# Performance work log

Measured on AMD Instinct MI355X. Metric: run time of the kernel, lower is better.

Reference implementation:

```python
import jax, jax.numpy as jnp
import numpy as np

N = 50000
E = 800000
DIN = 256
DH = 256
DOUT = 256
R = 8
B = 4


def setup_inputs() -> dict:
    key = jax.random.key(0)
    ks = jax.random.split(key, 12)
    s = 0.05
    return {
        "x": jax.random.normal(ks[0], (N, DIN), jnp.float32),
        "edge_index": jax.random.randint(ks[1], (2, E), 0, N, jnp.int64),
        "edge_type": jax.random.randint(ks[2], (E,), 0, R, jnp.int64),
        "basis1": jax.random.normal(ks[3], (B, DIN, DH), jnp.float32) * s,
        "comp1": jax.random.normal(ks[4], (R, B), jnp.float32) * s,
        "root1": jax.random.normal(ks[5], (DIN, DH), jnp.float32) * s,
        "bias1": jnp.zeros((DH,), jnp.float32),
        "basis2": jax.random.normal(ks[6], (B, DH, DOUT), jnp.float32) * s,
        "comp2": jax.random.normal(ks[7], (R, B), jnp.float32) * s,
        "root2": jax.random.normal(ks[8], (DH, DOUT), jnp.float32) * s,
        "bias2": jnp.zeros((DOUT,), jnp.float32),
    }


def rgcn_conv(x, src, dst, edge_type, basis, comp, root, bias):
    # Basis-decomposed relational conv (PyG RGCNConv, aggr='mean').
    # xb: per-node transform by each basis matrix -> [N, B, out]
    xb = jnp.einsum('ni,bio->nbo', x, basis)
    # Per-edge message: mix bases with relation coefficients -> [E, out]
    msg = jnp.einsum('eb,ebo->eo', comp[edge_type], xb[src])
    # Mean aggregation per (dst, relation): divide each edge by the count of
    # edges of its relation arriving at its destination, then scatter-add.
    key = dst * R + edge_type
    cnt = jax.ops.segment_sum(jnp.ones((msg.shape[0],), x.dtype), key,
                              num_segments=x.shape[0] * R)
    norm = 1.0 / jnp.maximum(cnt, 1.0)
    agg = jax.ops.segment_sum(msg * norm[key][:, None], dst,
                              num_segments=x.shape[0])
    return agg + x @ root + bias


def reference(x, edge_index, edge_type, basis1, comp1, root1, bias1,
              basis2, comp2, root2, bias2):
    src, dst = edge_index[0], edge_index[1]
    h = rgcn_conv(x, src, dst, edge_type, basis1, comp1, root1, bias1)
    h = jax.nn.relu(h)
    # dropout(p=0.4) is identity in eval mode
    out = rgcn_conv(h, src, dst, edge_type, basis2, comp2, root2, bias2)
    return out
```

## Files before the change

### kernel.cpp

```cpp
#include <hip/hip_runtime.h>
#include <hip/hip_bf16.h>

constexpr int N_NODES = 50000;
constexpr int N_EDGES = 800000;
constexpr int R_REL   = 8;
constexpr int BASES   = 4;
constexpr int D       = 256;
constexpr int KT      = BASES * D + D;

typedef __attribute__((ext_vector_type(8))) short bf16x8;
typedef __attribute__((ext_vector_type(4))) float f32x4;

__device__ inline float bfu_lo(unsigned u) { return __uint_as_float(u << 16); }
__device__ inline float bfu_hi(unsigned u) { return __uint_as_float(u & 0xFFFF0000u); }
__device__ inline unsigned short f2bu(float f) {
  __hip_bfloat16 h = __float2bfloat16(f);
  return *reinterpret_cast<unsigned short*>(&h);
}
__device__ inline void store_out(float* p, float v) { *p = v; }
__device__ inline void store_out(__hip_bfloat16* p, float v) { *p = __float2bfloat16(v); }

__device__ inline void gload_lds16(void* lds, const void* g) {
  __builtin_amdgcn_global_load_lds(
      (const __attribute__((address_space(1))) unsigned*)g,
      (__attribute__((address_space(3))) unsigned*)lds, 16, 0, 0);
}

__global__ __launch_bounds__(256) void count_kernel(
    const int* __restrict__ ei, const int* __restrict__ et,
    int* __restrict__ cnt) {
  int e = blockIdx.x * 256 + threadIdx.x;
  if (e < N_EDGES) {
    int dst = ei[N_EDGES + e];
    int rt  = et[e];
    atomicAdd(&cnt[dst * R_REL + rt], 1);
  }
}

__global__ __launch_bounds__(256) void scan_phaseA(
    const int* __restrict__ cnt, int* __restrict__ bsum) {
  __shared__ int sd[256];
  int tid = threadIdx.x;
  int n = blockIdx.x * 256 + tid;
  int d = 0;
  if (n < N_NODES) {
#pragma unroll
    for (int r = 0; r < R_REL; r++) d += cnt[n * R_REL + r];
  }
  sd[tid] = d;
  __syncthreads();
  for (int off = 128; off > 0; off >>= 1) {
    if (tid < off) sd[tid] += sd[tid + off];
    __syncthreads();
  }
  if (tid == 0) bsum[blockIdx.x] = sd[0];
}

__global__ __launch_bounds__(256) void scan_phaseB(
    const int* __restrict__ bsum, int* __restrict__ boff,
    int* __restrict__ estart, int NB) {
  __shared__ int sd[256];
  int tid = threadIdx.x;
  int v = (tid < NB) ? bsum[tid] : 0;
  sd[tid] = v;
  __syncthreads();
  for (int off = 1; off < 256; off <<= 1) {
    int t = (tid >= off) ? sd[tid - off] : 0;
    __syncthreads();
    sd[tid] += t;
    __syncthreads();
  }
  if (tid < NB) boff[tid] = sd[tid] - v;
  if (tid == 0) estart[N_NODES] = N_EDGES;
}

__global__ __launch_bounds__(256) void scan_phaseC(
    const int* __restrict__ cnt, const int* __restrict__ boff,
    int* __restrict__ estart) {
  __shared__ int sd[256];
  int tid = threadIdx.x;
  int n = blockIdx.x * 256 + tid;
  int d = 0;
  if (n < N_NODES) {
#pragma unroll
    for (int r = 0; r < R_REL; r++) d += cnt[n * R_REL + r];
  }
  sd[tid] = d;
  __syncthreads();
  for (int off = 1; off < 256; off <<= 1) {
    int t = (tid >= off) ? sd[tid - off] : 0;
    __syncthreads();
    sd[tid] += t;
    __syncthreads();
  }
  if (n < N_NODES) estart[n] = boff[blockIdx.x] + sd[tid] - d;
}

__global__ __launch_bounds__(256) void bucket_kernel(
    const int* __restrict__ ei, const int* __restrict__ et,
    const int* __restrict__ estart, int* __restrict__ cursor,
    int* __restrict__ packed) {
  int e = blockIdx.x * 256 + threadIdx.x;
  if (e < N_EDGES) {
    int src = ei[e];
    int dst = ei[N_EDGES + e];
    int rt  = et[e];
    int pos = estart[dst] + atomicAdd(&cursor[dst], 1);
    packed[pos] = src | (rt << 20);
  }
}

__global__ __launch_bounds__(256) void convert_kernel(
    const float* __restrict__ x, unsigned* __restrict__ x2) {
  int idx = blockIdx.x * 256 + threadIdx.x;
  if (idx < N_NODES * 128) {
    float2 v = *(const float2*)(x + (size_t)idx * 2);
    x2[idx] = (unsigned)f2bu(v.x) | ((unsigned)f2bu(v.y) << 16);
  }
}

__global__ __launch_bounds__(256) void winv_kernel(
    const int* __restrict__ cnt, const float* __restrict__ comp,
    float4* __restrict__ wtab) {
  int idx = blockIdx.x * 256 + threadIdx.x;
  if (idx < N_NODES * R_REL) {
    int r = idx & 7;
    int c = cnt[idx];
    float inv = 1.0f / (float)(c > 0 ? c : 1);
    float4 w;
    w.x = comp[r * BASES + 0] * inv;
    w.y = comp[r * BASES + 1] * inv;
    w.z = comp[r * BASES + 2] * inv;
    w.w = comp[r * BASES + 3] * inv;
    wtab[idx] = w;
  }
}

__global__ __launch_bounds__(256) void make_w_kernel(
    const float* __restrict__ basis, const float* __restrict__ root,
    __hip_bfloat16* __restrict__ WT) {
  __shared__ __hip_bfloat16 tile[64][256];
  int k0 = blockIdx.x * 64;
  int tid = threadIdx.x;
#pragma unroll 4
  for (int r = 0; r < 64; r++) {
    int k = k0 + r;
    const float* srow = (k < BASES * D)
        ? basis + ((size_t)(k & 3) * D + (k >> 2)) * D
        : root + (size_t)(k - BASES * D) * D;
    tile[r][tid] = __float2bfloat16(srow[tid]);
  }
  __syncthreads();
  __hip_bfloat16* dst = WT + (size_t)tid * KT + k0;
#pragma unroll
  for (int c = 0; c < 8; c++) {
    union { short s[8]; int4 v; } u;
#pragma unroll
    for (int r = 0; r < 8; r++)
      u.s[r] = *reinterpret_cast<short*>(&tile[c * 8 + r][tid]);
    *(int4*)(dst + c * 8) = u.v;
  }
}

__device__ inline void edge_fma(float acc[BASES][4], uint2 v, float4 w) {
  float a0 = bfu_lo(v.x), a1 = bfu_hi(v.x), a2 = bfu_lo(v.y), a3 = bfu_hi(v.y);
  acc[0][0] += w.x * a0; acc[0][1] += w.x * a1; acc[0][2] += w.x * a2; acc[0][3] += w.x * a3;
  acc[1][0] += w.y * a0; acc[1][1] += w.y * a1; acc[1][2] += w.y * a2; acc[1][3] += w.y * a3;
  acc[2][0] += w.z * a0; acc[2][1] += w.z * a1; acc[2][2] += w.z * a2; acc[2][3] += w.z * a3;
  acc[3][0] += w.w * a0; acc[3][1] += w.w * a1; acc[3][2] += w.w * a2; acc[3][3] += w.w * a3;
}

__global__ __launch_bounds__(256) void aggregate_kernel(
    const unsigned* __restrict__ x2,
    const int* __restrict__ packed,
    const int* __restrict__ estart,
    const float4* __restrict__ wtab,
    __hip_bfloat16* __restrict__ zA)
{
  int tid = threadIdx.x;
  int wave = tid >> 6, lane = tid & 63;
  int n = blockIdx.x * 4 + wave;
  const float4 wzero = make_float4(0.f, 0.f, 0.f, 0.f);

  float acc[BASES][4] = {};
  int s = estart[n], e = estart[n + 1];
  const float4* wt = wtab + (size_t)n * R_REL;

  for (int base = s; base < e; base += 4) {
    int rem = e - base;
    int i1 = base + (rem > 1 ? 1 : 0);
    int i2 = base + (rem > 2 ? 2 : 0);
    int i3 = base + (rem > 3 ? 3 : 0);
    int p0 = packed[base];
    int p1 = packed[i1];
    int p2 = packed[i2];
    int p3 = packed[i3];
    uint2 v0 = *(const uint2*)(x2 + (size_t)(p0 & 0xFFFFF) * 128 + lane * 2);
    uint2 v1 = *(const uint2*)(x2 + (size_t)(p1 & 0xFFFFF) * 128 + lane * 2);
    uint2 v2 = *(const uint2*)(x2 + (size_t)(p2 & 0xFFFFF) * 128 + lane * 2);
    uint2 v3 = *(const uint2*)(x2 + (size_t)(p3 & 0xFFFFF) * 128 + lane * 2);
    float4 w0 = wt[p0 >> 20];
    float4 w1 = (rem > 1) ? wt[p1 >> 20] : wzero;
    float4 w2 = (rem > 2) ? wt[p2 >> 20] : wzero;
    float4 w3 = (rem > 3) ? wt[p3 >> 20] : wzero;
    edge_fma(acc, v0, w0);
    edge_fma(acc, v1, w1);
    edge_fma(acc, v2, w2);
    edge_fma(acc, v3, w3);
  }

  union { short s[8]; int4 v; } u0, u1;
#pragma unroll
  for (int j = 0; j < 2; j++)
#pragma unroll
    for (int b = 0; b < BASES; b++) {
      u0.s[4 * j + b] = (short)f2bu(acc[b][j]);
      u1.s[4 * j + b] = (short)f2bu(acc[b][j + 2]);
    }
  __hip_bfloat16* zrow = zA + (size_t)n * KT;
  *(int4*)(zrow + 16 * lane) = u0.v;
  *(int4*)(zrow + 16 * lane + 8) = u1.v;

  uint2 sv = *(const uint2*)(x2 + (size_t)n * 128 + lane * 2);
  *(uint2*)((unsigned*)(zrow + BASES * D) + lane * 2) = sv;
}

#define BM 128
#define BN 256
#define BK 32

template <bool RELU, typename OutT>
__global__ __launch_bounds__(512) void gemm_kernel(
    const __hip_bfloat16* __restrict__ A,
    const __hip_bfloat16* __restrict__ Bt,
    const float* __restrict__ bias, OutT* __restrict__ C, int M) {
  __shared__ __align__(16) __hip_bfloat16 As[BM * BK];
  __shared__ __align__(16) __hip_bfloat16 Bs[BN * BK];
  int tid = threadIdx.x;
  int m0 = blockIdx.x * BM;
  int wave = tid >> 6, lane = tid & 63;
  int wm = wave & 1, wn = wave >> 1;
  int l15 = lane & 15, quad = lane >> 4;

  int colS = (lane & 3) * 8;
  int rowA = wave * 16 + (lane >> 2);
  int grA  = min(m0 + rowA, M - 1);
  const __hip_bfloat16* gA  = A + (size_t)grA * KT + colS;
  const __hip_bfloat16* gB0 = Bt + (size_t)(wave * 32 + (lane >> 2)) * KT + colS;
  const __hip_bfloat16* gB1 = gB0 + 16 * KT;
  __hip_bfloat16* lA  = As + wave * 512;
  __hip_bfloat16* lB0 = Bs + wave * 1024;
  __hip_bfloat16* lB1 = Bs + wave * 1024 + 512;

  f32x4 acc[4][4] = {};

  for (int k0 = 0; k0 < KT; k0 += BK) {
    gload_lds16(lA, gA + k0);
    gload_lds16(lB0, gB0 + k0);
    gload_lds16(lB1, gB1 + k0);
    __syncthreads();

    bf16x8 af[4], bfr[4];
#pragma unroll
    for (int mt = 0; mt < 4; mt++)
      af[mt] = *(const bf16x8*)(As + (wm * 64 + mt * 16 + l15) * BK + quad * 8);
#pragma unroll
    for (int nt = 0; nt < 4; nt++)
      bfr[nt] = *(const bf16x8*)(Bs + (wn * 64 + nt * 16 + l15) * BK + quad * 8);
#pragma unroll
    for (int mt = 0; mt < 4; mt++)
#pragma unroll
      for (int nt = 0; nt < 4; nt++)
        acc[mt][nt] = __builtin_amdgcn_mfma_f32_16x16x32_bf16(
            af[mt], bfr[nt], acc[mt][nt], 0, 0, 0);
    __syncthreads();
  }

#pragma unroll
  for (int nt = 0; nt < 4; nt++) {
    int cg = wn * 64 + nt * 16 + l15;
    float bv = bias[cg];
#pragma unroll
    for (int mt = 0; mt < 4; mt++) {
#pragma unroll
      for (int r = 0; r < 4; r++) {
        int rg = m0 + wm * 64 + mt * 16 + quad * 4 + r;
        if (rg < M) {
          float v = acc[mt][nt][r] + bv;
          if (RELU) v = fmaxf(v, 0.f);
          store_out(C + (size_t)rg * D + cg, v);
        }
      }
    }
  }
}

static inline char* carve(char*& p, size_t bytes) {
  char* r = p;
  p += (bytes + 255) & ~(size_t)255;
  return r;
}

extern "C" void kernel_launch(void* const* d_in, const int* in_sizes, int n_in,
                              void* d_out, int out_size, void* d_ws,
                              size_t ws_size, hipStream_t stream) {
  const float* x      = (const float*)d_in[0];
  const int*   ei     = (const int*)d_in[1];
  const int*   et     = (const int*)d_in[2];
  const float* basis1 = (const float*)d_in[3];
  const float* comp1  = (const float*)d_in[4];
  const float* root1  = (const float*)d_in[5];
  const float* bias1  = (const float*)d_in[6];
  const float* basis2 = (const float*)d_in[7];
  const float* comp2  = (const float*)d_in[8];
  const float* root2  = (const float*)d_in[9];
  const float* bias2  = (const float*)d_in[10];
  float* out = (float*)d_out;

  char* ws = (char*)d_ws;
  int* cnt    = (int*)carve(ws, (size_t)N_NODES * R_REL * 4);
  int* estart = (int*)carve(ws, (size_t)(N_NODES + 1) * 4);
  int* cursor = (int*)carve(ws, (size_t)N_NODES * 4);
  int* bsum   = (int*)carve(ws, 256 * 4);
  int* boff   = (int*)carve(ws, 256 * 4);
  int* packed = (int*)carve(ws, (size_t)N_EDGES * 4);
  float4* wtab1 = (float4*)carve(ws, (size_t)N_NODES * R_REL * 16);
  float4* wtab2 = (float4*)carve(ws, (size_t)N_NODES * R_REL * 16);
  __hip_bfloat16* WT1 = (__hip_bfloat16*)carve(ws, (size_t)D * KT * 2);
  __hip_bfloat16* WT2 = (__hip_bfloat16*)carve(ws, (size_t)D * KT * 2);
  unsigned* xb = (unsigned*)carve(ws, (size_t)N_NODES * D * 2);
  __hip_bfloat16* h = (__hip_bfloat16*)carve(ws, (size_t)N_NODES * D * 2);
  __hip_bfloat16* zA = (__hip_bfloat16*)carve(ws, (size_t)N_NODES * KT * 2);

  const int NB = (N_NODES + 255) / 256;
  const int EB = (N_EDGES + 255) / 256;
  const int CB = (N_NODES * 128 + 255) / 256;
  const int WB = (N_NODES * R_REL + 255) / 256;

  hipMemsetAsync(cnt, 0, (size_t)N_NODES * R_REL * 4, stream);
  hipMemsetAsync(cursor, 0, (size_t)N_NODES * 4, stream);

  count_kernel<<<EB, 256, 0, stream>>>(ei, et, cnt);
  scan_phaseA<<<NB, 256, 0, stream>>>(cnt, bsum);
  scan_phaseB<<<1, 256, 0, stream>>>(bsum, boff, estart, NB);
  scan_phaseC<<<NB, 256, 0, stream>>>(cnt, boff, estart);
  bucket_kernel<<<EB, 256, 0, stream>>>(ei, et, estart, cursor, packed);

  convert_kernel<<<CB, 256, 0, stream>>>(x, xb);
  winv_kernel<<<WB, 256, 0, stream>>>(cnt, comp1, wtab1);
  winv_kernel<<<WB, 256, 0, stream>>>(cnt, comp2, wtab2);
  make_w_kernel<<<KT / 64, 256, 0, stream>>>(basis1, root1, WT1);
  make_w_kernel<<<KT / 64, 256, 0, stream>>>(basis2, root2, WT2);

  dim3 ggrid((N_NODES + BM - 1) / BM, 1);
  const int AB = (N_NODES + 3) / 4;

  aggregate_kernel<<<AB, 256, 0, stream>>>(xb, packed, estart, wtab1, zA);
  gemm_kernel<true, __hip_bfloat16><<<ggrid, 512, 0, stream>>>(zA, WT1, bias1, h, N_NODES);

  aggregate_kernel<<<AB, 256, 0, stream>>>((const unsigned*)h, packed, estart, wtab2, zA);
  gemm_kernel<false, float><<<ggrid, 512, 0, stream>>>(zA, WT2, bias2, out, N_NODES);
}
```

Baseline: 498.4 us.

## Read self features directly in GEMM and use persistent work-stealing aggregation

The aggregation kernel no longer copies each node's own features into the concatenated A matrix. The GEMM instead reads the last K-slice straight from the node feature buffer, which removes a write and re-read of N×256 bf16 per layer. Aggregation becomes a persistent kernel: each wave takes a static chunk of nodes, then grabs more through an atomic counter, and the tail edges are handled by a scalar loop instead of masked duplicate loads. Outputs are written with nontemporal stores. This adds an atomic per chunk and a branch in the GEMM's A-pointer selection.

Result: slower. 729.5 us (+46.4%).

```diff
diff --git a/kernel.cpp b/kernel.cpp
--- a/kernel.cpp
+++ b/kernel.cpp
@@ -6,10 +6,12 @@
 constexpr int R_REL   = 8;
 constexpr int BASES   = 4;
 constexpr int D       = 256;
-constexpr int KT      = BASES * D + D;
+constexpr int KZ      = BASES * D;
+constexpr int KT      = KZ + D;
 
 typedef __attribute__((ext_vector_type(8))) short bf16x8;
 typedef __attribute__((ext_vector_type(4))) float f32x4;
+typedef __attribute__((ext_vector_type(4))) int   i32x4;
 
 __device__ inline float bfu_lo(unsigned u) { return __uint_as_float(u << 16); }
 __device__ inline float bfu_hi(unsigned u) { return __uint_as_float(u & 0xFFFF0000u); }
@@ -17,7 +19,7 @@
   __hip_bfloat16 h = __float2bfloat16(f);
   return *reinterpret_cast<unsigned short*>(&h);
 }
-__device__ inline void store_out(float* p, float v) { *p = v; }
+__device__ inline void store_out(float* p, float v) { __builtin_nontemporal_store(v, p); }
 __device__ inline void store_out(__hip_bfloat16* p, float v) { *p = __float2bfloat16(v); }
 
 __device__ inline void gload_lds16(void* lds, const void* g) {
@@ -145,9 +147,9 @@
 #pragma unroll 4
   for (int r = 0; r < 64; r++) {
     int k = k0 + r;
-    const float* srow = (k < BASES * D)
+    const float* srow = (k < KZ)
         ? basis + ((size_t)(k & 3) * D + (k >> 2)) * D
-        : root + (size_t)(k - BASES * D) * D;
+        : root + (size_t)(k - KZ) * D;
     tile[r][tid] = __float2bfloat16(srow[tid]);
   }
   __syncthreads();
@@ -162,12 +164,24 @@
   }
 }
 
-__device__ inline void edge_fma(float acc[BASES][4], uint2 v, float4 w) {
-  float a0 = bfu_lo(v.x), a1 = bfu_hi(v.x), a2 = bfu_lo(v.y), a3 = bfu_hi(v.y);
-  acc[0][0] += w.x * a0; acc[0][1] += w.x * a1; acc[0][2] += w.x * a2; acc[0][3] += w.x * a3;
-  acc[1][0] += w.y * a0; acc[1][1] += w.y * a1; acc[1][2] += w.y * a2; acc[1][3] += w.y * a3;
-  acc[2][0] += w.z * a0; acc[2][1] += w.z * a1; acc[2][2] += w.z * a2; acc[2][3] += w.z * a3;
-  acc[3][0] += w.w * a0; acc[3][1] += w.w * a1; acc[3][2] += w.w * a2; acc[3][3] += w.w * a3;
+constexpr int AGG_BLOCKS = 2048;
+constexpr int AGG_WAVES  = AGG_BLOCKS * 4;
+constexpr int GRAB       = 4;
+constexpr int NSTATIC    = AGG_WAVES * GRAB;
+
+__device__ inline float2 pfma(float s, float2 a, float2 c) {
+  c.x = fmaf(s, a.x, c.x);
+  c.y = fmaf(s, a.y, c.y);
+  return c;
+}
+
+__device__ inline void edge_fma(float2 acc[BASES][2], uint2 v, float4 w) {
+  float2 a01 = make_float2(bfu_lo(v.x), bfu_hi(v.x));
+  float2 a23 = make_float2(bfu_lo(v.y), bfu_hi(v.y));
+  acc[0][0] = pfma(w.x, a01, acc[0][0]); acc[0][1] = pfma(w.x, a23, acc[0][1]);
+  acc[1][0] = pfma(w.y, a01, acc[1][0]); acc[1][1] = pfma(w.y, a23, acc[1][1]);
+  acc[2][0] = pfma(w.z, a01, acc[2][0]); acc[2][1] = pfma(w.z, a23, acc[2][1]);
+  acc[3][0] = pfma(w.w, a01, acc[3][0]); acc[3][1] = pfma(w.w, a23, acc[3][1]);
 }
 
 __global__ __launch_bounds__(256) void aggregate_kernel(
@@ -175,54 +189,66 @@
     const int* __restrict__ packed,
     const int* __restrict__ estart,
     const float4* __restrict__ wtab,
-    __hip_bfloat16* __restrict__ zA)
+    __hip_bfloat16* __restrict__ zA,
+    int* __restrict__ wq)
 {
-  int tid = threadIdx.x;
+  int tid  = threadIdx.x;
   int wave = tid >> 6, lane = tid & 63;
-  int n = blockIdx.x * 4 + wave;
-  const float4 wzero = make_float4(0.f, 0.f, 0.f, 0.f);
-
-  float acc[BASES][4] = {};
-  int s = estart[n], e = estart[n + 1];
-  const float4* wt = wtab + (size_t)n * R_REL;
-
-  for (int base = s; base < e; base += 4) {
-    int rem = e - base;
-    int i1 = base + (rem > 1 ? 1 : 0);
-    int i2 = base + (rem > 2 ? 2 : 0);
-    int i3 = base + (rem > 3 ? 3 : 0);
-    int p0 = packed[base];
-    int p1 = packed[i1];
-    int p2 = packed[i2];
-    int p3 = packed[i3];
-    uint2 v0 = *(const uint2*)(x2 + (size_t)(p0 & 0xFFFFF) * 128 + lane * 2);
-    uint2 v1 = *(const uint2*)(x2 + (size_t)(p1 & 0xFFFFF) * 128 + lane * 2);
-    uint2 v2 = *(const uint2*)(x2 + (size_t)(p2 & 0xFFFFF) * 128 + lane * 2);
-    uint2 v3 = *(const uint2*)(x2 + (size_t)(p3 & 0xFFFFF) * 128 + lane * 2);
-    float4 w0 = wt[p0 >> 20];
-    float4 w1 = (rem > 1) ? wt[p1 >> 20] : wzero;
-    float4 w2 = (rem > 2) ? wt[p2 >> 20] : wzero;
-    float4 w3 = (rem > 3) ? wt[p3 >> 20] : wzero;
-    edge_fma(acc, v0, w0);
-    edge_fma(acc, v1, w1);
-    edge_fma(acc, v2, w2);
-    edge_fma(acc, v3, w3);
-  }
-
-  union { short s[8]; int4 v; } u0, u1;
-#pragma unroll
-  for (int j = 0; j < 2; j++)
-#pragma unroll
-    for (int b = 0; b < BASES; b++) {
-      u0.s[4 * j + b] = (short)f2bu(acc[b][j]);
-      u1.s[4 * j + b] = (short)f2bu(acc[b][j + 2]);
+  int nbase = (blockIdx.x * 4 + wave) * GRAB;
+
+  while (nbase < N_NODES) {
+    int nend = nbase + GRAB;
+    if (nend > N_NODES) nend = N_NODES;
+
+    for (int n = nbase; n < nend; n++) {
+      float2 acc[BASES][2] = {};
+      int s = estart[n], e = estart[n + 1];
+      const float4* wt = wtab + (size_t)n * R_REL;
+
+      int i = s;
+      for (; i + 4 <= e; i += 4) {
+        int p0 = packed[i];
+        int p1 = packed[i + 1];
+        int p2 = packed[i + 2];
+        int p3 = packed[i + 3];
+        uint2 v0 = *(const uint2*)(x2 + (size_t)(p0 & 0xFFFFF) * 128 + lane * 2);
+        uint2 v1 = *(const uint2*)(x2 + (size_t)(p1 & 0xFFFFF) * 128 + lane * 2);
+        uint2 v2 = *(const uint2*)(x2 + (size_t)(p2 & 0xFFFFF) * 128 + lane * 2);
+        uint2 v3 = *(const uint2*)(x2 + (size_t)(p3 & 0xFFFFF) * 128 + lane * 2);
+        float4 w0 = wt[p0 >> 20];
+        float4 w1 = wt[p1 >> 20];
+        float4 w2 = wt[p2 >> 20];
+        float4 w3 = wt[p3 >> 20];
+        edge_fma(acc, v0, w0);
+        edge_fma(acc, v1, w1);
+        edge_fma(acc, v2, w2);
+        edge_fma(acc, v3, w3);
+      }
+      for (; i < e; i++) {
+        int p = packed[i];
+        uint2 v = *(const uint2*)(x2 + (size_t)(p & 0xFFFFF) * 128 + lane * 2);
+        float4 w = wt[p >> 20];
+        edge_fma(acc, v, w);
+      }
+
+      union { short s[8]; i32x4 v; } u0, u1;
+#pragma unroll
+      for (int b = 0; b < BASES; b++) {
+        u0.s[b]     = (short)f2bu(acc[b][0].x);
+        u0.s[4 + b] = (short)f2bu(acc[b][0].y);
+        u1.s[b]     = (short)f2bu(acc[b][1].x);
+        u1.s[4 + b] = (short)f2bu(acc[b][1].y);
+      }
+      __hip_bfloat16* zrow = zA + (size_t)n * KZ;
+      __builtin_nontemporal_store(u0.v, (i32x4*)(zrow + 16 * lane));
+      __builtin_nontemporal_store(u1.v, (i32x4*)(zrow + 16 * lane + 8));
     }
-  __hip_bfloat16* zrow = zA + (size_t)n * KT;
-  *(int4*)(zrow + 16 * lane) = u0.v;
-  *(int4*)(zrow + 16 * lane + 8) = u1.v;
-
-  uint2 sv = *(const uint2*)(x2 + (size_t)n * 128 + lane * 2);
-  *(uint2*)((unsigned*)(zrow + BASES * D) + lane * 2) = sv;
+
+    int idx0 = 0;
+    if (lane == 0) idx0 = atomicAdd(wq, 1);
+    int idx = __builtin_amdgcn_readfirstlane(idx0);
+    nbase = NSTATIC + idx * GRAB;
+  }
 }
 
 #define BM 128
@@ -231,7 +257,8 @@
 
 template <bool RELU, typename OutT>
 __global__ __launch_bounds__(512) void gemm_kernel(
-    const __hip_bfloat16* __restrict__ A,
+    const __hip_bfloat16* __restrict__ Az,
+    const __hip_bfloat16* __restrict__ Aself,
     const __hip_bfloat16* __restrict__ Bt,
     const float* __restrict__ bias, OutT* __restrict__ C, int M) {
   __shared__ __align__(16) __hip_bfloat16 As[BM * BK];
@@ -245,7 +272,8 @@
   int colS = (lane & 3) * 8;
   int rowA = wave * 16 + (lane >> 2);
   int grA  = min(m0 + rowA, M - 1);
-  const __hip_bfloat16* gA  = A + (size_t)grA * KT + colS;
+  const __hip_bfloat16* gAz = Az + (size_t)grA * KZ + colS;
+  const __hip_bfloat16* gAs = Aself + (size_t)grA * D + colS;
   const __hip_bfloat16* gB0 = Bt + (size_t)(wave * 32 + (lane >> 2)) * KT + colS;
   const __hip_bfloat16* gB1 = gB0 + 16 * KT;
   __hip_bfloat16* lA  = As + wave * 512;
@@ -255,7 +283,8 @@
   f32x4 acc[4][4] = {};
 
   for (int k0 = 0; k0 < KT; k0 += BK) {
-    gload_lds16(lA, gA + k0);
+    const __hip_bfloat16* srcA = (k0 < KZ) ? (gAz + k0) : (gAs + (k0 - KZ));
+    gload_lds16(lA, srcA);
     gload_lds16(lB0, gB0 + k0);
     gload_lds16(lB1, gB1 + k0);
     __syncthreads();
@@ -323,6 +352,7 @@
   int* cursor = (int*)carve(ws, (size_t)N_NODES * 4);
   int* bsum   = (int*)carve(ws, 256 * 4);
   int* boff   = (int*)carve(ws, 256 * 4);
+  int* wq     = (int*)carve(ws, 2 * 4);
   int* packed = (int*)carve(ws, (size_t)N_EDGES * 4);
   float4* wtab1 = (float4*)carve(ws, (size_t)N_NODES * R_REL * 16);
   float4* wtab2 = (float4*)carve(ws, (size_t)N_NODES * R_REL * 16);
@@ -330,7 +360,7 @@
   __hip_bfloat16* WT2 = (__hip_bfloat16*)carve(ws, (size_t)D * KT * 2);
   unsigned* xb = (unsigned*)carve(ws, (size_t)N_NODES * D * 2);
   __hip_bfloat16* h = (__hip_bfloat16*)carve(ws, (size_t)N_NODES * D * 2);
-  __hip_bfloat16* zA = (__hip_bfloat16*)carve(ws, (size_t)N_NODES * KT * 2);
+  __hip_bfloat16* zA = (__hip_bfloat16*)carve(ws, (size_t)N_NODES * KZ * 2);
 
   const int NB = (N_NODES + 255) / 256;
   const int EB = (N_EDGES + 255) / 256;
@@ -339,6 +369,7 @@
 
   hipMemsetAsync(cnt, 0, (size_t)N_NODES * R_REL * 4, stream);
   hipMemsetAsync(cursor, 0, (size_t)N_NODES * 4, stream);
+  hipMemsetAsync(wq, 0, 2 * 4, stream);
 
   count_kernel<<<EB, 256, 0, stream>>>(ei, et, cnt);
   scan_phaseA<<<NB, 256, 0, stream>>>(cnt, bsum);
@@ -353,11 +384,14 @@
   make_w_kernel<<<KT / 64, 256, 0, stream>>>(basis2, root2, WT2);
 
   dim3 ggrid((N_NODES + BM - 1) / BM, 1);
-  const int AB = (N_NODES + 3) / 4;
-
-  aggregate_kernel<<<AB, 256, 0, stream>>>(xb, packed, estart, wtab1, zA);
-  gemm_kernel<true, __hip_bfloat16><<<ggrid, 512, 0, stream>>>(zA, WT1, bias1, h, N_NODES);
-
-  aggregate_kernel<<<AB, 256, 0, stream>>>((const unsigned*)h, packed, estart, wtab2, zA);
-  gemm_kernel<false, float><<<ggrid, 512, 0, stream>>>(zA, WT2, bias2, out, N_NODES);
-}
+
+  aggregate_kernel<<<AGG_BLOCKS, 256, 0, stream>>>(xb, packed, estart, wtab1,
+                                                   zA, wq);
+  gemm_kernel<true, __hip_bfloat16><<<ggrid, 512, 0, stream>>>(
+      zA, (const __hip_bfloat16*)xb, WT1, bias1, h, N_NODES);
+
+  aggregate_kernel<<<AGG_BLOCKS, 256, 0, stream>>>((const unsigned*)h, packed,
+                                                   estart, wtab2, zA, wq + 1);
+  gemm_kernel<false, float><<<ggrid, 512, 0, stream>>>(
+      zA, h, WT2, bias2, out, N_NODES);
+}
```
